# Performance work log

Measured on AMD Instinct MI355X. Metric: run time of the kernel, lower is better.

The kernel has to match this reference:

```python
import jax, jax.numpy as jnp
import numpy as np

VEC = 512
HEADS = 8
HEAD = VEC // HEADS  # 64
B, L = 4, 2048
EPS = 1e-3  # keras LayerNormalization default epsilon


def setup_inputs() -> dict:
    key = jax.random.key(0)
    ks = jax.random.split(key, 9)
    return {
        "query": jax.random.normal(ks[0], (B, L, VEC), dtype=jnp.float32),
        "key": jax.random.normal(ks[1], (B, L, VEC), dtype=jnp.float32),
        "value": jax.random.normal(ks[2], (B, L, VEC), dtype=jnp.float32),
        "query_mask": jnp.ones((B, L), dtype=jnp.float32),
        "value_mask": jnp.ones((B, L), dtype=jnp.float32),
        "Wq": jax.random.normal(ks[3], (HEADS, VEC, HEAD), dtype=jnp.float32) * 0.02,
        "Wk": jax.random.normal(ks[4], (HEADS, VEC, HEAD), dtype=jnp.float32) * 0.02,
        "Wv": jax.random.normal(ks[5], (HEADS, VEC, HEAD), dtype=jnp.float32) * 0.02,
        "gamma": jnp.ones((VEC,), dtype=jnp.float32),
        "beta": jnp.zeros((VEC,), dtype=jnp.float32),
    }


def reference(query, key, value, query_mask, value_mask, Wq, Wk, Wv, gamma, beta):
    b, l, v = query.shape
    h, _, d = Wq.shape
    # batched per-head projections (equivalent to the per-head Dense loop)
    Q = jnp.einsum("blv,hvd->bhld", query, Wq)
    K = jnp.einsum("blv,hvd->bhld", key, Wk)
    V = jnp.einsum("blv,hvd->bhld", value, Wv)
    scores = jnp.einsum("bhld,bhmd->bhlm", Q, K) / jnp.sqrt(jnp.float32(d))
    att = jax.nn.softmax(scores, axis=-1)
    # post-softmax multiplicative masks (faithful to the original)
    tri = jnp.tril(jnp.ones((l, l), dtype=att.dtype))  # causal triangle mask
    att = att * tri
    att = att * (query_mask[:, None, :, None] * value_mask[:, None, None, :])
    head = jnp.einsum("bhlm,bhmd->bhld", att, V)
    # concat heads along feature dim: (B,L,H*D)
    x = jnp.transpose(head, (0, 2, 1, 3)).reshape(b, l, h * d)
    # dropout inactive at inference; residual + LayerNorm (eps=1e-3)
    y = x + query
    mean = jnp.mean(y, axis=-1, keepdims=True)
    var = jnp.mean(jnp.square(y - mean), axis=-1, keepdims=True)
    return (y - mean) / jnp.sqrt(var + EPS) * gamma + beta
```

## Files before the change

### kernel.cpp

```cpp
#include <hip/hip_runtime.h>
#include <hip/hip_bf16.h>

#define BSZ 4
#define LSEQ 2048
#define VECD 512
#define NH 8
#define HD 64

typedef __attribute__((ext_vector_type(8))) short bf16x8;
typedef __attribute__((ext_vector_type(4))) short short4v;
typedef __attribute__((ext_vector_type(8))) short short8v;
typedef __attribute__((ext_vector_type(4))) float f32x4;
typedef __attribute__((ext_vector_type(16))) float f32x16;

__device__ inline short f2bf(float f) {
    union { float f; unsigned u; } v; v.f = f;
    unsigned u = v.u;
    u += 0x7fffu + ((u >> 16) & 1u);
    return (short)(u >> 16);
}

__device__ inline unsigned cvtpk_bf16(float lo, float hi) {
    unsigned r;
    asm volatile("v_cvt_pk_bf16_f32 %0, %1, %2" : "=v"(r) : "v"(lo), "v"(hi));
    return r;
}

__device__ inline float exp2a(float v) {
    float r;
    asm("v_exp_f32 %0, %1" : "=v"(r) : "v"(v));
    return r;
}

__device__ inline void plswap(unsigned &a, unsigned &b) {
    asm volatile("v_permlane32_swap_b32 %0, %1" : "+v"(a), "+v"(b));
}

__device__ inline void gll16(const void* g, void* l) {
    __builtin_amdgcn_global_load_lds(
        (const __attribute__((address_space(1))) unsigned int*)g,
        (__attribute__((address_space(3))) unsigned int*)l, 16, 0, 0);
}

__launch_bounds__(256)
__global__ void w_kernel(const float* __restrict__ Wq, const float* __restrict__ Wk,
                         const float* __restrict__ Wv, short* __restrict__ WT) {
    __shared__ short T[64][72];
    const int bi = blockIdx.x;
    const int z = bi >> 3, h = bi & 7;
    const float* W = ((z == 0) ? Wq : (z == 1) ? Wk : Wv) + (size_t)h * VECD * HD;
    short* out = WT + (size_t)z * 512 * 512 + (size_t)h * 64 * 512;

    const int tid = threadIdx.x;
    for (int kt = 0; kt < 8; kt++) {
        int k0 = kt * 64;
        int r = tid >> 2, seg = tid & 3;
        for (int j = 0; j < 4; j++) {
            float4 v = *(const float4*)(W + (size_t)(k0 + r) * HD + seg * 16 + j * 4);
            T[seg * 16 + j * 4 + 0][r] = f2bf(v.x);
            T[seg * 16 + j * 4 + 1][r] = f2bf(v.y);
            T[seg * 16 + j * 4 + 2][r] = f2bf(v.z);
            T[seg * 16 + j * 4 + 3][r] = f2bf(v.w);
        }
        __syncthreads();
        int d = tid >> 2, ks = tid & 3;
        *(short8v*)(out + (size_t)d * 512 + k0 + ks * 16) = *(const short8v*)&T[d][ks * 16];
        *(short8v*)(out + (size_t)d * 512 + k0 + ks * 16 + 8) = *(const short8v*)&T[d][ks * 16 + 8];
        __syncthreads();
    }
}

__launch_bounds__(256, 3)
__global__ void proj_kernel(const float* __restrict__ q_in, const float* __restrict__ k_in,
                            const float* __restrict__ v_in, const short* __restrict__ WT,
                            short* __restrict__ Qp, short* __restrict__ Kp,
                            short* __restrict__ Vp) {
    __shared__ short As[128 * 64];
    __shared__ short Bs[128 * 64];

    const int id    = blockIdx.x;
    const int xcd   = id & 7;
    const int local = id >> 3;
    const int n0i   = local & 3;
    const int pl    = local >> 2;
    const int gp    = xcd * 24 + pl;
    const int z     = gp >> 6;
    const int xb    = gp & 63;

    const float* in = (z == 0) ? q_in : (z == 1) ? k_in : v_in;
    short* out      = (z == 0) ? Qp   : (z == 1) ? Kp   : Vp;
    const float sc  = (z == 0) ? 0.18033688011112042f : 1.0f;
    const short* wt = WT + (size_t)z * 512 * 512;

    const int tid  = threadIdx.x;
    const int lane = tid & 63;
    const int w    = tid >> 6;
    const int r0   = xb * 128;
    const int n0   = n0i * 128;

    const int row16 = lane & 15;
    const int grp   = lane >> 4;
    const int wm    = (w >> 1) * 64;
    const int wn    = (w & 1) * 64;

    f32x4 acc[4][4];
    for (int i = 0; i < 4; i++)
        for (int j = 0; j < 4; j++) acc[i][j] = (f32x4)0.f;

    for (int k0 = 0; k0 < VECD; k0 += 64) {
        for (int i = 0; i < 8; i++) {
            int id2 = tid + 256 * i;
            int m = id2 >> 4, kc4 = id2 & 15;
            float4 v = *(const float4*)(in + (size_t)(r0 + m) * VECD + k0 + kc4 * 4);
            int c = kc4 >> 1, half = kc4 & 1;
            uint2 p;
            p.x = cvtpk_bf16(v.x, v.y);
            p.y = cvtpk_bf16(v.z, v.w);
            *(uint2*)&As[m * 64 + (c ^ (m & 7)) * 8 + half * 4] = p;
        }
        for (int i = 0; i < 4; i++) {
            int id2 = tid + 256 * i;
            int n = id2 >> 3, c = id2 & 7;
            gll16(wt + (size_t)(n0 + n) * 512 + k0 + ((c ^ (n & 7)) * 8),
                  (void*)(Bs + (w * 64 + 256 * i) * 8));
        }
        __syncthreads();

        for (int kc = 0; kc < 2; kc++) {
            bf16x8 a[4], b[4];
            for (int mt = 0; mt < 4; mt++) {
                int row = wm + mt * 16 + row16;
                int cg = kc * 4 + grp;
                a[mt] = *(const bf16x8*)&As[row * 64 + (cg ^ (row & 7)) * 8];
            }
            for (int nt = 0; nt < 4; nt++) {
                int row = wn + nt * 16 + row16;
                int cg = kc * 4 + grp;
                b[nt] = *(const bf16x8*)&Bs[row * 64 + (cg ^ (row & 7)) * 8];
            }
            for (int mt = 0; mt < 4; mt++)
                for (int nt = 0; nt < 4; nt++)
                    acc[mt][nt] = __builtin_amdgcn_mfma_f32_16x16x32_bf16(a[mt], b[nt], acc[mt][nt], 0, 0, 0);
        }
        __syncthreads();
    }

    for (int mt = 0; mt < 4; mt++)
        for (int r = 0; r < 4; r++) {
            int m = r0 + wm + mt * 16 + grp * 4 + r;
            int b = m >> 11, l = m & (LSEQ - 1);
            for (int nt = 0; nt < 4; nt++) {
                int n = n0 + wn + nt * 16 + row16;
                int h = n >> 6, d = n & 63;
                out[(((size_t)b * NH + h) * LSEQ + l) * HD + d] = f2bf(acc[mt][nt][r] * sc);
            }
        }
}

__launch_bounds__(256)
__global__ void vt_kernel(const short* __restrict__ Vp, short* __restrict__ VpT) {
    __shared__ short T[64][72];
    const int bh = blockIdx.y;
    const int l0 = blockIdx.x * 64;
    const short* src = Vp + (size_t)bh * LSEQ * HD + (size_t)l0 * HD;
    short* dst = VpT + (size_t)bh * HD * LSEQ;

    const int tid = threadIdx.x;
    const int row = tid >> 2, c16 = tid & 3;
    *(bf16x8*)&T[row][c16 * 16]     = *(const bf16x8*)(src + row * HD + c16 * 16);
    *(bf16x8*)&T[row][c16 * 16 + 8] = *(const bf16x8*)(src + row * HD + c16 * 16 + 8);
    __syncthreads();

    const int d = tid >> 2, seg = tid & 3;
    short8v o0, o1;
    for (int j = 0; j < 8; j++) o0[j] = T[seg * 16 + j][d];
    for (int j = 0; j < 8; j++) o1[j] = T[seg * 16 + 8 + j][d];
    *(short8v*)(dst + (size_t)d * LSEQ + l0 + seg * 16)     = o0;
    *(short8v*)(dst + (size_t)d * LSEQ + l0 + seg * 16 + 8) = o1;
}

__launch_bounds__(256, 4)
__global__ void attn_kernel(const short* __restrict__ Qp, const short* __restrict__ Kp,
                            const short* __restrict__ VpT,
                            const float* __restrict__ qmask, const float* __restrict__ vmask,
                            short* __restrict__ x) {
    __shared__ char smem[16384 + 2 * 2 * 32 * 4];
    short* Ks  = (short*)smem;
    short* VTs = (short*)(smem + 8192);
    float* Dd  = (float*)(smem + 16384);
    float* Ex  = (float*)smem;

    const int tid  = threadIdx.x;
    const int lane = tid & 63;
    const int w    = tid >> 6;
    const int pair = w >> 1;
    const int mh   = w & 1;

    const int ii  = blockIdx.x + 32 * blockIdx.y;
    const int swz = (ii & 7) * 128 + (ii >> 3);
    const int x31 = swz & 31;
    const int bh  = swz >> 5;
    const int b   = bh >> 3;
    const int h   = bh & 7;

    const int t  = (pair == 0) ? x31 : (63 - x31);
    const int kd = t >> 1;
    const int kv = (63 - x31) >> 1;
    const int qbase = t * 32;

    const size_t base   = (size_t)bh * LSEQ * HD;
    const size_t vtbase = (size_t)bh * HD * LSEQ;

    const int l31  = lane & 31;
    const int hsel = lane >> 5;
    const int lq   = qbase + l31;

    bf16x8 q[4];
    #pragma unroll
    for (int ks = 0; ks < 4; ks++)
        q[ks] = *(const bf16x8*)(Qp + base + (size_t)lq * HD + ks * 16 + hsel * 8);

    f32x16 o0 = (f32x16)0.f, o1 = (f32x16)0.f;
    float dsum = 0.f;

    bf16x8 kr[2], vr[2];
    auto loadTile = [&](int k) {
        const short* ksrc = Kp + base + (size_t)(k * 64) * HD;
        #pragma unroll
        for (int i = 0; i < 2; i++) {
            int id = tid + 256 * i;
            int row = id >> 3, c = id & 7;
            int cs = c ^ (row & 7) ^ ((row >> 3) & 7);
            kr[i] = *(const bf16x8*)(ksrc + row * HD + cs * 8);
            if (k <= kv)
                vr[i] = *(const bf16x8*)(VpT + vtbase + (size_t)row * LSEQ + k * 64 + cs * 8);
        }
    };
    auto writeTile = [&](int k) {
        #pragma unroll
        for (int i = 0; i < 2; i++) {
            int id = tid + 256 * i;
            *(bf16x8*)&Ks[id * 8] = kr[i];
            if (k <= kv) *(bf16x8*)&VTs[id * 8] = vr[i];
        }
    };

    loadTile(0);
    writeTile(0);

    const int mrow = mh * 32 + l31;
    const int msw  = (mrow & 7) ^ ((mrow >> 3) & 7);

    for (int k = 0; k < 32; ++k) {
        __syncthreads();
        if (k < 31) loadTile(k + 1);

        f32x16 s = (f32x16)0.f;
        bf16x8 kf[4];
        #pragma unroll
        for (int ks = 0; ks < 4; ks++)
            kf[ks] = *(const bf16x8*)&Ks[mrow * 64 + ((ks * 2 + hsel) ^ msw) * 8];
        #pragma unroll
        for (int ks = 0; ks < 4; ks++)
            s = __builtin_amdgcn_mfma_f32_32x32x16_bf16(kf[ks], q[ks], s, 0, 0, 0);

        float e[16];
        #pragma unroll
        for (int r = 0; r < 16; r++) {
            e[r] = exp2a(s[r]);
            dsum += e[r];
        }

        if (k <= kd) {
            #pragma unroll
            for (int g = 0; g < 4; g++) {
                int mb = k * 64 + mh * 32 + 8 * g + 4 * hsel;
                float4 vm = *(const float4*)(vmask + b * LSEQ + mb);
                float m0v = vm.x, m1v = vm.y, m2v = vm.z, m3v = vm.w;
                if (k == kd) {
                    m0v = (mb + 0 <= lq) ? m0v : 0.f;
                    m1v = (mb + 1 <= lq) ? m1v : 0.f;
                    m2v = (mb + 2 <= lq) ? m2v : 0.f;
                    m3v = (mb + 3 <= lq) ? m3v : 0.f;
                }
                e[4 * g + 0] *= m0v; e[4 * g + 1] *= m1v;
                e[4 * g + 2] *= m2v; e[4 * g + 3] *= m3v;
            }

            #pragma unroll
            for (int ks2 = 0; ks2 < 2; ks2++) {
                int b0 = 8 * ks2;
                unsigned pk0 = cvtpk_bf16(e[b0 + 0], e[b0 + 1]);
                unsigned pk1 = cvtpk_bf16(e[b0 + 2], e[b0 + 3]);
                unsigned pk2 = cvtpk_bf16(e[b0 + 4], e[b0 + 5]);
                unsigned pk3 = cvtpk_bf16(e[b0 + 6], e[b0 + 7]);
                plswap(pk2, pk0);
                plswap(pk3, pk1);
                union { unsigned u[4]; bf16x8 v; } pu;
                pu.u[0] = pk0; pu.u[1] = pk1; pu.u[2] = pk2; pu.u[3] = pk3;

                int chunk = mh * 4 + ks2 * 2 + hsel;
                {
                    int drow = l31;
                    bf16x8 vb = *(const bf16x8*)&VTs[drow * 64 +
                        ((chunk ^ (drow & 7) ^ ((drow >> 3) & 7))) * 8];
                    o0 = __builtin_amdgcn_mfma_f32_32x32x16_bf16(pu.v, vb, o0, 0, 0, 0);
                }
                {
                    int drow = 32 + l31;
                    bf16x8 vb = *(const bf16x8*)&VTs[drow * 64 +
                        ((chunk ^ (drow & 7) ^ ((drow >> 3) & 7))) * 8];
                    o1 = __builtin_amdgcn_mfma_f32_32x32x16_bf16(pu.v, vb, o1, 0, 0, 0);
                }
            }
        }

        __syncthreads();
        if (k < 31) writeTile(k + 1);
    }

    dsum += __shfl_xor(dsum, 32, 64);
    if (lane < 32) Dd[pair * 64 + mh * 32 + l31] = dsum;
    __syncthreads();

    {
        const int wbuf = (pair * 2 + (1 - mh)) * 1024;
        #pragma unroll
        for (int r = 0; r < 16; r++) {
            int ql = (r & 3) + 8 * (r >> 2) + 4 * hsel;
            Ex[wbuf + ql * 32 + l31] = (mh == 0) ? o1[r] : o0[r];
        }
    }
    __syncthreads();

    {
        const int rbuf = (pair * 2 + mh) * 1024;
        #pragma unroll
        for (int r = 0; r < 16; r++) {
            int ql = (r & 3) + 8 * (r >> 2) + 4 * hsel;
            float own = (mh == 0) ? o0[r] : o1[r];
            float val = own + Ex[rbuf + ql * 32 + l31];
            float den = Dd[pair * 64 + ql] + Dd[pair * 64 + 32 + ql];
            int lqr = qbase + ql;
            float inv = qmask[b * LSEQ + lqr] / den;
            x[((size_t)b * LSEQ + lqr) * VECD + h * HD + mh * 32 + l31] = f2bf(val * inv);
        }
    }
}

__launch_bounds__(256)
__global__ void ln_kernel(const short* __restrict__ x, const float* __restrict__ q,
                          const float* __restrict__ gamma, const float* __restrict__ beta,
                          float* __restrict__ out) {
    const int tid  = threadIdx.x;
    const int lane = tid & 63;
    const int w    = tid >> 6;
    const size_t row = (size_t)blockIdx.x * 4 + w;

    short8v xs = *(const short8v*)(x + row * VECD + lane * 8);
    const float* qr = q + row * VECD + lane * 8;
    float4 b0 = *(const float4*)qr;
    float4 b1 = *(const float4*)(qr + 4);
    float xb[8];
    #pragma unroll
    for (int j = 0; j < 8; j++) {
        union { unsigned u; float f; } c; c.u = ((unsigned)(unsigned short)xs[j]) << 16;
        xb[j] = c.f;
    }
    float y[8] = { xb[0] + b0.x, xb[1] + b0.y, xb[2] + b0.z, xb[3] + b0.w,
                   xb[4] + b1.x, xb[5] + b1.y, xb[6] + b1.z, xb[7] + b1.w };

    float s = 0.f;
    for (int j = 0; j < 8; j++) s += y[j];
    for (int off = 1; off < 64; off <<= 1) s += __shfl_xor(s, off, 64);
    float mean = s * (1.f / 512.f);

    float v = 0.f;
    for (int j = 0; j < 8; j++) { float d = y[j] - mean; v += d * d; }
    for (int off = 1; off < 64; off <<= 1) v += __shfl_xor(v, off, 64);
    float inv = rsqrtf(v * (1.f / 512.f) + 1e-3f);

    float4 g0 = *(const float4*)(gamma + lane * 8);
    float4 g1 = *(const float4*)(gamma + lane * 8 + 4);
    float4 e0 = *(const float4*)(beta + lane * 8);
    float4 e1 = *(const float4*)(beta + lane * 8 + 4);

    float4 o0, o1;
    o0.x = (y[0] - mean) * inv * g0.x + e0.x;
    o0.y = (y[1] - mean) * inv * g0.y + e0.y;
    o0.z = (y[2] - mean) * inv * g0.z + e0.z;
    o0.w = (y[3] - mean) * inv * g0.w + e0.w;
    o1.x = (y[4] - mean) * inv * g1.x + e1.x;
    o1.y = (y[5] - mean) * inv * g1.y + e1.y;
    o1.z = (y[6] - mean) * inv * g1.z + e1.z;
    o1.w = (y[7] - mean) * inv * g1.w + e1.w;
    *(float4*)(out + row * VECD + lane * 8) = o0;
    *(float4*)(out + row * VECD + lane * 8 + 4) = o1;
}

extern "C" void kernel_launch(void* const* d_in, const int* in_sizes, int n_in,
                              void* d_out, int out_size, void* d_ws, size_t ws_size,
                              hipStream_t stream) {
    const float* query = (const float*)d_in[0];
    const float* key   = (const float*)d_in[1];
    const float* value = (const float*)d_in[2];
    const float* qmask = (const float*)d_in[3];
    const float* vmask = (const float*)d_in[4];
    const float* Wq    = (const float*)d_in[5];
    const float* Wk    = (const float*)d_in[6];
    const float* Wv    = (const float*)d_in[7];
    const float* gamma = (const float*)d_in[8];
    const float* beta  = (const float*)d_in[9];

    const size_t QKV_ELTS = (size_t)BSZ * NH * LSEQ * HD;
    short* Qp = (short*)d_ws;
    short* Kp = Qp + QKV_ELTS;
    short* Vp = Kp + QKV_ELTS;
    short* x  = Vp + QKV_ELTS;
    short* WT = x + QKV_ELTS;
    short* VpT = WT + (size_t)3 * 512 * 512;

    w_kernel<<<24, 256, 0, stream>>>(Wq, Wk, Wv, WT);
    proj_kernel<<<768, 256, 0, stream>>>(query, key, value, WT, Qp, Kp, Vp);
    vt_kernel<<<dim3(32, 32), 256, 0, stream>>>(Vp, VpT);
    attn_kernel<<<dim3(32, 32), 256, 0, stream>>>(Qp, Kp, VpT, qmask, vmask, x);
    ln_kernel<<<2048, 256, 0, stream>>>(x, query, gamma, beta, (float*)d_out);
}
```

Baseline: 106.7 us.

## Fuse V transpose into projection epilogue and double-buffer attention tiles via direct LDS loads

The projection kernel now writes V already transposed, staging the tile through shared memory, so the separate vt_kernel launch and its extra round trip through global memory are gone. The attention kernel swaps register-staged K/V tile loads for global-to-LDS direct loads (gll16) into two shared-memory buffers, dropping one barrier per iteration. This doubles attention LDS use, which may lower occupancy, and the proj kernel gains an extra barrier and LDS staging for the V blocks.

```diff
diff --git a/kernel.cpp b/kernel.cpp
--- a/kernel.cpp
+++ b/kernel.cpp
@@ -74,9 +74,11 @@
 __global__ void proj_kernel(const float* __restrict__ q_in, const float* __restrict__ k_in,
                             const float* __restrict__ v_in, const short* __restrict__ WT,
                             short* __restrict__ Qp, short* __restrict__ Kp,
-                            short* __restrict__ Vp) {
-    __shared__ short As[128 * 64];
-    __shared__ short Bs[128 * 64];
+                            short* __restrict__ VpT) {
+    __shared__ char psm[128 * 136 * 2];
+    short* As = (short*)psm;
+    short* Bs = As + 128 * 64;
+    short* T  = (short*)psm;
 
     const int id    = blockIdx.x;
     const int xcd   = id & 7;
@@ -88,7 +90,6 @@
     const int xb    = gp & 63;
 
     const float* in = (z == 0) ? q_in : (z == 1) ? k_in : v_in;
-    short* out      = (z == 0) ? Qp   : (z == 1) ? Kp   : Vp;
     const float sc  = (z == 0) ? 0.18033688011112042f : 1.0f;
     const short* wt = WT + (size_t)z * 512 * 512;
 
@@ -145,38 +146,38 @@
         __syncthreads();
     }
 
-    for (int mt = 0; mt < 4; mt++)
-        for (int r = 0; r < 4; r++) {
-            int m = r0 + wm + mt * 16 + grp * 4 + r;
-            int b = m >> 11, l = m & (LSEQ - 1);
-            for (int nt = 0; nt < 4; nt++) {
-                int n = n0 + wn + nt * 16 + row16;
-                int h = n >> 6, d = n & 63;
-                out[(((size_t)b * NH + h) * LSEQ + l) * HD + d] = f2bf(acc[mt][nt][r] * sc);
-            }
-        }
-}
-
-__launch_bounds__(256)
-__global__ void vt_kernel(const short* __restrict__ Vp, short* __restrict__ VpT) {
-    __shared__ short T[64][72];
-    const int bh = blockIdx.y;
-    const int l0 = blockIdx.x * 64;
-    const short* src = Vp + (size_t)bh * LSEQ * HD + (size_t)l0 * HD;
-    short* dst = VpT + (size_t)bh * HD * LSEQ;
-
-    const int tid = threadIdx.x;
-    const int row = tid >> 2, c16 = tid & 3;
-    *(bf16x8*)&T[row][c16 * 16]     = *(const bf16x8*)(src + row * HD + c16 * 16);
-    *(bf16x8*)&T[row][c16 * 16 + 8] = *(const bf16x8*)(src + row * HD + c16 * 16 + 8);
-    __syncthreads();
-
-    const int d = tid >> 2, seg = tid & 3;
-    short8v o0, o1;
-    for (int j = 0; j < 8; j++) o0[j] = T[seg * 16 + j][d];
-    for (int j = 0; j < 8; j++) o1[j] = T[seg * 16 + 8 + j][d];
-    *(short8v*)(dst + (size_t)d * LSEQ + l0 + seg * 16)     = o0;
-    *(short8v*)(dst + (size_t)d * LSEQ + l0 + seg * 16 + 8) = o1;
+    if (z == 2) {
+        for (int mt = 0; mt < 4; mt++)
+            for (int r = 0; r < 4; r++) {
+                int ml = wm + mt * 16 + grp * 4 + r;
+                for (int nt = 0; nt < 4; nt++) {
+                    int nl = wn + nt * 16 + row16;
+                    T[nl * 136 + ml] = f2bf(acc[mt][nt][r]);
+                }
+            }
+        __syncthreads();
+        const int nl = tid >> 1, half = tid & 1;
+        const int n = n0 + nl;
+        const int h = n >> 6, d = n & 63;
+        const int b = r0 >> 11;
+        const int lbase = (r0 & (LSEQ - 1)) + half * 64;
+        short* dst = VpT + (((size_t)b * NH + h) * HD + d) * LSEQ + lbase;
+        #pragma unroll
+        for (int j = 0; j < 8; j++)
+            *(short8v*)(dst + j * 8) = *(const short8v*)&T[nl * 136 + half * 64 + j * 8];
+    } else {
+        short* out = (z == 0) ? Qp : Kp;
+        for (int mt = 0; mt < 4; mt++)
+            for (int r = 0; r < 4; r++) {
+                int m = r0 + wm + mt * 16 + grp * 4 + r;
+                int b = m >> 11, l = m & (LSEQ - 1);
+                for (int nt = 0; nt < 4; nt++) {
+                    int n = n0 + wn + nt * 16 + row16;
+                    int h = n >> 6, d = n & 63;
+                    out[(((size_t)b * NH + h) * LSEQ + l) * HD + d] = f2bf(acc[mt][nt][r] * sc);
+                }
+            }
+    }
 }
 
 __launch_bounds__(256, 4)
@@ -184,11 +185,9 @@
                             const short* __restrict__ VpT,
                             const float* __restrict__ qmask, const float* __restrict__ vmask,
                             short* __restrict__ x) {
-    __shared__ char smem[16384 + 2 * 2 * 32 * 4];
-    short* Ks  = (short*)smem;
-    short* VTs = (short*)(smem + 8192);
-    float* Dd  = (float*)(smem + 16384);
-    float* Ex  = (float*)smem;
+    __shared__ char smem[2 * 16384 + 2 * 2 * 32 * 4];
+    float* Dd = (float*)(smem + 32768);
+    float* Ex = (float*)smem;
 
     const int tid  = threadIdx.x;
     const int lane = tid & 63;
@@ -223,37 +222,34 @@
     f32x16 o0 = (f32x16)0.f, o1 = (f32x16)0.f;
     float dsum = 0.f;
 
-    bf16x8 kr[2], vr[2];
-    auto loadTile = [&](int k) {
+    auto stage = [&](int k, int buf) {
         const short* ksrc = Kp + base + (size_t)(k * 64) * HD;
+        short* Ksb = (short*)(smem + buf * 16384);
+        short* VTb = Ksb + 4096;
         #pragma unroll
         for (int i = 0; i < 2; i++) {
             int id = tid + 256 * i;
             int row = id >> 3, c = id & 7;
             int cs = c ^ (row & 7) ^ ((row >> 3) & 7);
-            kr[i] = *(const bf16x8*)(ksrc + row * HD + cs * 8);
+            gll16(ksrc + row * HD + cs * 8, (void*)(Ksb + (w * 64 + 256 * i) * 8));
             if (k <= kv)
-                vr[i] = *(const bf16x8*)(VpT + vtbase + (size_t)row * LSEQ + k * 64 + cs * 8);
+                gll16(VpT + vtbase + (size_t)row * LSEQ + k * 64 + cs * 8,
+                      (void*)(VTb + (w * 64 + 256 * i) * 8));
         }
     };
-    auto writeTile = [&](int k) {
-        #pragma unroll
-        for (int i = 0; i < 2; i++) {
-            int id = tid + 256 * i;
-            *(bf16x8*)&Ks[id * 8] = kr[i];
-            if (k <= kv) *(bf16x8*)&VTs[id * 8] = vr[i];
-        }
-    };
-
-    loadTile(0);
-    writeTile(0);
+
+    stage(0, 0);
 
     const int mrow = mh * 32 + l31;
     const int msw  = (mrow & 7) ^ ((mrow >> 3) & 7);
 
+    int cur = 0;
     for (int k = 0; k < 32; ++k) {
         __syncthreads();
-        if (k < 31) loadTile(k + 1);
+        if (k < 31) stage(k + 1, cur ^ 1);
+
+        const short* Ks  = (const short*)(smem + cur * 16384);
+        const short* VTs = Ks + 4096;
 
         f32x16 s = (f32x16)0.f;
         bf16x8 kf[4];
@@ -315,8 +311,7 @@
             }
         }
 
-        __syncthreads();
-        if (k < 31) writeTile(k + 1);
+        cur ^= 1;
     }
 
     dsum += __shfl_xor(dsum, 32, 64);
@@ -413,16 +408,14 @@
     const float* beta  = (const float*)d_in[9];
 
     const size_t QKV_ELTS = (size_t)BSZ * NH * LSEQ * HD;
-    short* Qp = (short*)d_ws;
-    short* Kp = Qp + QKV_ELTS;
-    short* Vp = Kp + QKV_ELTS;
-    short* x  = Vp + QKV_ELTS;
-    short* WT = x + QKV_ELTS;
-    short* VpT = WT + (size_t)3 * 512 * 512;
+    short* Qp  = (short*)d_ws;
+    short* Kp  = Qp + QKV_ELTS;
+    short* VpT = Kp + QKV_ELTS;
+    short* x   = VpT + QKV_ELTS;
+    short* WT  = x + QKV_ELTS;
 
     w_kernel<<<24, 256, 0, stream>>>(Wq, Wk, Wv, WT);
-    proj_kernel<<<768, 256, 0, stream>>>(query, key, value, WT, Qp, Kp, Vp);
-    vt_kernel<<<dim3(32, 32), 256, 0, stream>>>(Vp, VpT);
+    proj_kernel<<<768, 256, 0, stream>>>(query, key, value, WT, Qp, Kp, VpT);
     attn_kernel<<<dim3(32, 32), 256, 0, stream>>>(Qp, Kp, VpT, qmask, vmask, x);
     ln_kernel<<<2048, 256, 0, stream>>>(x, query, gamma, beta, (float*)d_out);
 }
```

New measurement: 104.3 us. -2.3%, faster.
